# Optimization experiments

Measured on AMD Instinct MI355X. Metric: run time of the kernel, lower is better.

The kernel has to match this reference:

```python
import jax, jax.numpy as jnp
import numpy as np

B, S, D = 2, 2048, 1024
H, DK, DV = 16, 64, 64
D_OUT = 1024


def setup_inputs() -> dict:
    key = jax.random.key(0)
    ks = jax.random.split(key, 9)
    sd = 1.0 / np.sqrt(D)
    # Linear weights stored as [in, out] (torch applies x @ W.T with W [out,in])
    return {
        "x": jax.random.normal(ks[0], (B, S, D), dtype=jnp.float32),
        "Wq": jax.random.normal(ks[1], (D, H * DK), dtype=jnp.float32) * sd,
        "bq": jnp.zeros((H * DK,), dtype=jnp.float32),
        "Wk": jax.random.normal(ks[2], (D, H * DK), dtype=jnp.float32) * sd,
        "bk": jnp.zeros((H * DK,), dtype=jnp.float32),
        "Wv": jax.random.normal(ks[3], (D, H * DV), dtype=jnp.float32) * sd,
        "bv": jnp.zeros((H * DV,), dtype=jnp.float32),
        "Wo": jax.random.normal(ks[4], (H * DV, D_OUT), dtype=jnp.float32) * sd,
        "bo": jnp.zeros((D_OUT,), dtype=jnp.float32),
    }


def _attn(x, Wq, bq, Wk, bk, Wv, bv, Wo, bo):
    n = x.shape[-2]
    q = (x @ Wq + bq).reshape(B, n, H, DK).transpose(0, 2, 1, 3)  # [B,H,S,DK]
    k = (x @ Wk + bk).reshape(B, n, H, DK).transpose(0, 2, 1, 3)
    v = (x @ Wv + bv).reshape(B, n, H, DV).transpose(0, 2, 1, 3)
    scores = jnp.einsum("bhqd,bhkd->bhqk", q / jnp.sqrt(jnp.float32(DK)), k)
    # causal additive mask: 0 on/below diagonal, -inf above (matches 1 - 1/tril)
    causal = jnp.tril(jnp.ones((n, n), dtype=bool))
    scores = jnp.where(causal, scores, -jnp.inf)
    probs = jax.nn.softmax(scores, axis=-1)
    out = jnp.einsum("bhqk,bhkd->bhqd", probs, v)  # [B,H,S,DV]
    out = out.transpose(0, 2, 1, 3).reshape(B, n, H * DV)
    return out @ Wo + bo


def reference(x, Wq, bq, Wk, bk, Wv, bv, Wo, bo):
    return _attn(x, Wq, bq, Wk, bk, Wv, bv, Wo, bo)
```

## Files before the change

### kernel.cpp

```cpp
#include <hip/hip_runtime.h>

typedef unsigned short u16;
typedef __bf16 bf16_t;
typedef bf16_t bf16x8 __attribute__((ext_vector_type(8)));
typedef float f32x4 __attribute__((ext_vector_type(4)));

#define DEV __device__ __forceinline__
#define LOG2E 1.4426950408889634f
#define QKS (0.125f * LOG2E)

static_assert(sizeof(bf16x8) == 16, "bf16x8 must be 16B");

DEV u16 f2b(float v) { return __builtin_bit_cast(u16, (bf16_t)v); }
DEV float b2f(u16 v) { return (float)__builtin_bit_cast(bf16_t, v); }

DEV void g2l16(const void* g, void* l) {
  __builtin_amdgcn_global_load_lds(
      (const __attribute__((address_space(1))) void*)g,
      (__attribute__((address_space(3))) void*)l, 16, 0, 0);
}

DEV int sniff_is_f32(const u16* __restrict__ W) {
  const int lane = threadIdx.x & 63;
  int cnt = 0;
#pragma unroll
  for (int i = 0; i < 8; i++) {
    u16 u = W[(lane * 8 + i) * 2];
    cnt += (((u >> 7) & 0xFF) >= 126) ? 1 : 0;
  }
#pragma unroll
  for (int off = 1; off < 64; off <<= 1) cnt += __shfl_xor(cnt, off, 64);
  return cnt > 128;
}


__global__ __launch_bounds__(256) void convert_x_k(
    const void* __restrict__ xin, const u16* __restrict__ Wsniff,
    u16* __restrict__ xb) {
  const int i = (blockIdx.x * 256 + threadIdx.x) * 8;
  if (sniff_is_f32(Wsniff)) {
    const float* xf = (const float*)xin;
    float4 a = *(const float4*)&xf[i];
    float4 b = *(const float4*)&xf[i + 4];
    u16 o[8] = {f2b(a.x), f2b(a.y), f2b(a.z), f2b(a.w),
                f2b(b.x), f2b(b.y), f2b(b.z), f2b(b.w)};
    *(uint4*)&xb[i] = *(const uint4*)o;
  } else {
    *(uint4*)&xb[i] = *(const uint4*)((const u16*)xin + i);
  }
}

__global__ __launch_bounds__(256) void transpose_k(
    const void* __restrict__ Wq, const void* __restrict__ Wk,
    const void* __restrict__ Wv, const void* __restrict__ Wo,
    const void* __restrict__ bq, const void* __restrict__ bk,
    const void* __restrict__ bv, const void* __restrict__ bo,
    u16* __restrict__ Wqkv_t, u16* __restrict__ Wo_t,
    u16* __restrict__ bqkv_b, u16* __restrict__ bo_b) {
  __shared__ u16 tile[64][68];
  const int z = blockIdx.z;
  const void* src = (z == 0) ? Wq : (z == 1) ? Wk : (z == 2) ? Wv : Wo;
  u16* dst = (z < 3) ? (Wqkv_t + (size_t)z * 1024 * 1024) : Wo_t;
  const int k0 = blockIdx.y * 64, n0 = blockIdx.x * 64;
  const int t = threadIdx.x;
  const int r = t >> 4, c4 = (t & 15) * 4;
  const int isf = sniff_is_f32((const u16*)Wq);

  if (blockIdx.x == 0 && blockIdx.y == 0) {
    const void* bsrc = (z == 0) ? bq : (z == 1) ? bk : (z == 2) ? bv : bo;
    u16* bdst = (z < 3) ? (bqkv_b + z * 1024) : bo_b;
#pragma unroll
    for (int i = 0; i < 4; i++) {
      const int idx = t + i * 256;
      const float v =
          isf ? ((const float*)bsrc)[idx] : b2f(((const u16*)bsrc)[idx]);
      bdst[idx] = f2b(v);
    }
  }

#pragma unroll
  for (int i = 0; i < 4; i++) {
    int rr = r + i * 16;
    const size_t base = (size_t)(k0 + rr) * 1024 + n0 + c4;
    if (isf) {
      float4 v = *(const float4*)((const float*)src + base);
      tile[rr][c4] = f2b(v.x); tile[rr][c4 + 1] = f2b(v.y);
      tile[rr][c4 + 2] = f2b(v.z); tile[rr][c4 + 3] = f2b(v.w);
    } else {
      ushort4 v = *(const ushort4*)((const u16*)src + base);
      tile[rr][c4] = v.x; tile[rr][c4 + 1] = v.y;
      tile[rr][c4 + 2] = v.z; tile[rr][c4 + 3] = v.w;
    }
  }
  __syncthreads();
#pragma unroll
  for (int i = 0; i < 4; i++) {
    int rr = r + i * 16;
    ushort4 v;
    v.x = tile[c4][rr]; v.y = tile[c4 + 1][rr];
    v.z = tile[c4 + 2][rr]; v.w = tile[c4 + 3][rr];
    *(ushort4*)&dst[(size_t)(n0 + rr) * 1024 + k0 + c4] = v;
  }
}

template <int MODE>
__global__ __launch_bounds__(256, 3) void gemm_k(
    const u16* __restrict__ A, const u16* __restrict__ Bt,
    const u16* __restrict__ bias, void* __restrict__ o0v,
    u16* __restrict__ o1, u16* __restrict__ o2,
    const u16* __restrict__ Wsniff, int M, int N, int K) {
  alignas(16) __shared__ u16 As[128][32];
  alignas(16) __shared__ u16 Bs[128][32];
  const int tid = threadIdx.x;
  const int wave = tid >> 6, lane = tid & 63;
  const int quad = lane >> 4, l16 = lane & 15;
  const int m0 = blockIdx.y * 128, n0 = blockIdx.x * 128;
  const int wr = (wave >> 1) * 64, wc = (wave & 1) * 64;

  f32x4 acc[4][4];
#pragma unroll
  for (int i = 0; i < 4; i++)
#pragma unroll
    for (int j = 0; j < 4; j++) acc[i][j] = (f32x4){0.f, 0.f, 0.f, 0.f};

  const int srow = lane >> 2, scol = (lane & 3) * 8;
  for (int k0 = 0; k0 < K; k0 += 32) {
    __syncthreads();
#pragma unroll
    for (int j = 0; j < 4; j++) {
      const int t = wave * 4 + j;
      if (t < 8) {
        const int row = t * 16 + srow;
        g2l16(&A[(size_t)(m0 + row) * K + k0 + scol], &As[t * 16][0]);
      } else {
        const int rb = t - 8;
        const int row = rb * 16 + srow;
        g2l16(&Bt[(size_t)(n0 + row) * K + k0 + scol], &Bs[rb * 16][0]);
      }
    }
    __syncthreads();
    bf16x8 af[4], bfr[4];
#pragma unroll
    for (int mi = 0; mi < 4; mi++)
      af[mi] = *(const bf16x8*)&As[wr + mi * 16 + l16][quad * 8];
#pragma unroll
    for (int ni = 0; ni < 4; ni++)
      bfr[ni] = *(const bf16x8*)&Bs[wc + ni * 16 + l16][quad * 8];
#pragma unroll
    for (int mi = 0; mi < 4; mi++)
#pragma unroll
      for (int ni = 0; ni < 4; ni++)
        acc[mi][ni] = __builtin_amdgcn_mfma_f32_16x16x32_bf16(
            af[mi], bfr[ni], acc[mi][ni], 0, 0, 0);
  }

  const int isf = (MODE == 1) ? sniff_is_f32(Wsniff) : 0;
#pragma unroll
  for (int mi = 0; mi < 4; mi++) {
    const int rbase = m0 + wr + mi * 16 + quad * 4;
#pragma unroll
    for (int ni = 0; ni < 4; ni++) {
      const int col = n0 + wc + ni * 16 + l16;
      const float bv_ = b2f(bias[col]);
      if (MODE == 0) {
        const int seg = col >> 10;
        const int nn = col & 1023;
        const int h = nn >> 6, d = nn & 63;
        u16* op = (seg == 0) ? (u16*)o0v : (seg == 1) ? o1 : o2;
#pragma unroll
        for (int r = 0; r < 4; r++) {
          const int m = rbase + r;
          const int b = m >> 11, s = m & 2047;
          float v = acc[mi][ni][r] + bv_;
          if (seg == 0) v *= QKS;
          if (seg < 2)
            op[(((size_t)(b * 16 + h) * 2048) + s) * 64 + d] = f2b(v);
          else
            op[(((size_t)(b * 16 + h) * 64) + d) * 2048 + s] = f2b(v);
        }
      } else {
#pragma unroll
        for (int r = 0; r < 4; r++) {
          const int m = rbase + r;
          const float v = acc[mi][ni][r] + bv_;
          if (isf) ((float*)o0v)[(size_t)m * N + col] = v;
          else     ((u16*)o0v)[(size_t)m * N + col] = f2b(v);
        }
      }
    }
  }
}

__global__ __launch_bounds__(512, 4) void attn_k(
    const u16* __restrict__ Q, const u16* __restrict__ K,
    const u16* __restrict__ Vt, u16* __restrict__ O) {
  alignas(16) __shared__ u16 Ks[2][128][64];
  alignas(16) __shared__ u16 Vs[2][64][128];
  alignas(16) __shared__ u16 PsT[128][64];
  const int tid = threadIdx.x;
  const int w = tid >> 6, lane = tid & 63;
  const int quad = lane >> 4, l16 = lane & 15;
  const int bh = blockIdx.y;
  const int b = bh >> 4, h = bh & 15;
  const int sw = l16 & 7;

  const int krow_off = lane >> 3, kchunk = lane & 7;
  const int vrow_off = lane >> 4, vchunk = lane & 15;

  for (int pi = 0; pi < 2; pi++) {
    const int qt = pi ? (15 - (int)blockIdx.x) : (int)blockIdx.x;
    const int q0 = qt * 128;
    const int wrow = q0 + w * 16;
    const int nkt = qt + 1;

    bf16x8 aq[2];
#pragma unroll
    for (int kc = 0; kc < 2; kc++)
      aq[kc] = *(const bf16x8*)&Q[((size_t)bh * 2048 + wrow + l16) * 64 +
                                  kc * 32 + quad * 8];

    f32x4 oacc[4];
#pragma unroll
    for (int di = 0; di < 4; di++) oacc[di] = (f32x4){0.f, 0.f, 0.f, 0.f};
    float lrp = 0.f;

    auto stage = [&](int buf, int kts) {
      const int k0s = kts * 128;
#pragma unroll
      for (int j = 0; j < 4; j++) {
        const int t = w * 4 + j;
        if (t < 16) {
          const int r = t * 8 + krow_off;
          const int cs = kchunk ^ (r & 7);
          g2l16(&K[((size_t)bh * 2048 + k0s + r) * 64 + cs * 8],
                &Ks[buf][t * 8][0]);
        } else {
          const int t2 = t - 16;
          const int r = t2 * 4 + vrow_off;
          const int cs = vchunk ^ (r & 7);
          g2l16(&Vt[((size_t)bh * 64 + r) * 2048 + k0s + cs * 8],
                &Vs[buf][t2 * 4][0]);
        }
      }
    };

    stage(0, 0);
    for (int kt = 0; kt < nkt; kt++) {
      const int cur = kt & 1;
      const int k0 = kt * 128;
      if (kt + 1 < nkt) {
        stage(cur ^ 1, kt + 1);
        asm volatile("s_waitcnt vmcnt(4)" ::: "memory");
      } else {
        asm volatile("s_waitcnt vmcnt(0)" ::: "memory");
      }
      asm volatile("s_barrier" ::: "memory");

#pragma unroll
      for (int h2 = 0; h2 < 2; h2++) {
        const int k0h = k0 + h2 * 64;
        if (k0h > wrow + 15) continue;
        const bool needmask = (k0h + 63 > wrow);

        f32x4 st[4];
#pragma unroll
        for (int nk = 0; nk < 4; nk++) st[nk] = (f32x4){0.f, 0.f, 0.f, 0.f};
#pragma unroll
        for (int kc = 0; kc < 2; kc++)
#pragma unroll
          for (int nk = 0; nk < 4; nk++) {
            const int pos = ((kc << 2) | quad) ^ sw;
            bf16x8 kf =
                *(const bf16x8*)&Ks[cur][h2 * 64 + nk * 16 + l16][pos * 8];
            st[nk] = __builtin_amdgcn_mfma_f32_16x16x32_bf16(kf, aq[kc],
                                                             st[nk], 0, 0, 0);
          }

        const int q_glob = wrow + l16;
#pragma unroll
        for (int nk = 0; nk < 4; nk++) {
          const int kbase = k0h + nk * 16 + quad * 4;
          u16 pk[4];
#pragma unroll
          for (int r = 0; r < 4; r++) {
            float p = __builtin_amdgcn_exp2f(st[nk][r]);
            if (needmask && (kbase + r > q_glob)) p = 0.f;
            lrp += p;
            pk[r] = f2b(p);
          }
          const int g = nk * 4 + quad;
          const int cc = (g >> 1) ^ sw;
          *(uint2*)&PsT[w * 16 + l16][cc * 8 + (g & 1) * 4] =
              *(const uint2*)pk;
        }
        asm volatile("s_waitcnt lgkmcnt(0)" ::: "memory");

#pragma unroll
        for (int kc = 0; kc < 2; kc++) {
          const int pcc = ((kc << 2) | quad) ^ sw;
          bf16x8 ap = *(const bf16x8*)&PsT[w * 16 + l16][pcc * 8];
#pragma unroll
          for (int di = 0; di < 4; di++) {
            const int pos = ((h2 << 3) | (kc << 2) | quad) ^ sw;
            bf16x8 vf = *(const bf16x8*)&Vs[cur][di * 16 + l16][pos * 8];
            oacc[di] = __builtin_amdgcn_mfma_f32_16x16x32_bf16(ap, vf,
                                                               oacc[di], 0, 0, 0);
          }
        }
      }
      asm volatile("s_barrier" ::: "memory");
    }

    lrp += __shfl_xor(lrp, 16, 64);
    lrp += __shfl_xor(lrp, 32, 64);
    float rdiv[4];
#pragma unroll
    for (int r = 0; r < 4; r++) rdiv[r] = __shfl(lrp, quad * 4 + r, 64);

#pragma unroll
    for (int di = 0; di < 4; di++)
#pragma unroll
      for (int r = 0; r < 4; r++) {
        const int row = wrow + quad * 4 + r;
        const float v = oacc[di][r] / rdiv[r];
        O[((size_t)b * 2048 + row) * 1024 + h * 64 + di * 16 + l16] = f2b(v);
      }
  }
}

extern "C" void kernel_launch(void* const* d_in, const int* in_sizes, int n_in,
                              void* d_out, int out_size, void* d_ws,
                              size_t ws_size, hipStream_t stream) {
  const void* x  = d_in[0];
  const void* Wq = d_in[1];
  const void* bq = d_in[2];
  const void* Wk = d_in[3];
  const void* bk = d_in[4];
  const void* Wv = d_in[5];
  const void* bv = d_in[6];
  const void* Wo = d_in[7];
  const void* bo = d_in[8];

  char* ws = (char*)d_ws;
  u16* xb     = (u16*)ws;          ws += (size_t)4096 * 1024 * 2;
  u16* Wqkv_t = (u16*)ws;          ws += (size_t)3072 * 1024 * 2;
  u16* Wo_t   = (u16*)ws;          ws += (size_t)1024 * 1024 * 2;
  u16* bqkv_b = (u16*)ws;          ws += 3072 * 2;
  u16* bo_b   = (u16*)ws;          ws += 1024 * 2 + 128;
  u16* Qb     = (u16*)ws;          ws += (size_t)4096 * 1024 * 2;
  u16* Kb     = (u16*)ws;          ws += (size_t)4096 * 1024 * 2;
  u16* Vtb    = (u16*)ws;          ws += (size_t)4096 * 1024 * 2;
  u16* Ob     = xb;

  convert_x_k<<<2048, 256, 0, stream>>>(x, (const u16*)Wq, xb);
  transpose_k<<<dim3(16, 16, 4), 256, 0, stream>>>(Wq, Wk, Wv, Wo, bq, bk, bv,
                                                   bo, Wqkv_t, Wo_t, bqkv_b,
                                                   bo_b);
  gemm_k<0><<<dim3(24, 32), 256, 0, stream>>>(xb, Wqkv_t, bqkv_b, Qb, Kb, Vtb,
                                              (const u16*)Wq, 4096, 3072, 1024);
  attn_k<<<dim3(8, 32), 512, 0, stream>>>(Qb, Kb, Vtb, Ob);
  gemm_k<1><<<dim3(8, 32), 256, 0, stream>>>(Ob, Wo_t, bo_b, d_out, nullptr,
                                             nullptr, (const u16*)Wq, 4096,
                                             1024, 1024);
}
```

Measured before the change: 210.6 us.

## Split attention KV tiles across two blocks, widen GEMM K-step, stage V transpose

The attention kernel now splits each query tile's key tiles between two blocks, alternating even and odd tiles. Each block writes unnormalized partial outputs and row sums, and a new norm kernel combines and normalizes them. This doubles the grid, giving more parallelism for the causal workload, at the cost of an extra kernel launch and extra global traffic for the partials. Separately, the GEMM now uses a 64-wide K step with swizzled LDS, and the V-transposed epilogue is staged through shared memory so the global stores are coalesced.

```diff
diff --git a/kernel.cpp b/kernel.cpp
--- a/kernel.cpp
+++ b/kernel.cpp
@@ -109,13 +109,15 @@
     const u16* __restrict__ bias, void* __restrict__ o0v,
     u16* __restrict__ o1, u16* __restrict__ o2,
     const u16* __restrict__ Wsniff, int M, int N, int K) {
-  alignas(16) __shared__ u16 As[128][32];
-  alignas(16) __shared__ u16 Bs[128][32];
+  alignas(16) __shared__ u16 smem[2][128][64];
+  u16(*As)[64] = smem[0];
+  u16(*Bs)[64] = smem[1];
   const int tid = threadIdx.x;
   const int wave = tid >> 6, lane = tid & 63;
   const int quad = lane >> 4, l16 = lane & 15;
   const int m0 = blockIdx.y * 128, n0 = blockIdx.x * 128;
   const int wr = (wave >> 1) * 64, wc = (wave & 1) * 64;
+  const int sw = l16 & 7;
 
   f32x4 acc[4][4];
 #pragma unroll
@@ -123,35 +125,76 @@
 #pragma unroll
     for (int j = 0; j < 4; j++) acc[i][j] = (f32x4){0.f, 0.f, 0.f, 0.f};
 
-  const int srow = lane >> 2, scol = (lane & 3) * 8;
-  for (int k0 = 0; k0 < K; k0 += 32) {
+  const int srow = lane >> 3, schunk = lane & 7;
+  const int cs = schunk ^ srow;
+
+  for (int k0 = 0; k0 < K; k0 += 64) {
     __syncthreads();
 #pragma unroll
-    for (int j = 0; j < 4; j++) {
-      const int t = wave * 4 + j;
-      if (t < 8) {
-        const int row = t * 16 + srow;
-        g2l16(&A[(size_t)(m0 + row) * K + k0 + scol], &As[t * 16][0]);
+    for (int j = 0; j < 8; j++) {
+      const int t = wave * 8 + j;
+      if (t < 16) {
+        const int row = t * 8 + srow;
+        g2l16(&A[(size_t)(m0 + row) * K + k0 + cs * 8], &As[t * 8][0]);
       } else {
-        const int rb = t - 8;
-        const int row = rb * 16 + srow;
-        g2l16(&Bt[(size_t)(n0 + row) * K + k0 + scol], &Bs[rb * 16][0]);
+        const int t2 = t - 16;
+        const int row = t2 * 8 + srow;
+        g2l16(&Bt[(size_t)(n0 + row) * K + k0 + cs * 8], &Bs[t2 * 8][0]);
       }
     }
     __syncthreads();
-    bf16x8 af[4], bfr[4];
-#pragma unroll
-    for (int mi = 0; mi < 4; mi++)
-      af[mi] = *(const bf16x8*)&As[wr + mi * 16 + l16][quad * 8];
-#pragma unroll
-    for (int ni = 0; ni < 4; ni++)
-      bfr[ni] = *(const bf16x8*)&Bs[wc + ni * 16 + l16][quad * 8];
-#pragma unroll
-    for (int mi = 0; mi < 4; mi++)
+#pragma unroll
+    for (int kk = 0; kk < 2; kk++) {
+      const int pos = ((kk << 2) | quad) ^ sw;
+      bf16x8 af[4], bfr[4];
+#pragma unroll
+      for (int mi = 0; mi < 4; mi++)
+        af[mi] = *(const bf16x8*)&As[wr + mi * 16 + l16][pos * 8];
 #pragma unroll
       for (int ni = 0; ni < 4; ni++)
-        acc[mi][ni] = __builtin_amdgcn_mfma_f32_16x16x32_bf16(
-            af[mi], bfr[ni], acc[mi][ni], 0, 0, 0);
+        bfr[ni] = *(const bf16x8*)&Bs[wc + ni * 16 + l16][pos * 8];
+#pragma unroll
+      for (int mi = 0; mi < 4; mi++)
+#pragma unroll
+        for (int ni = 0; ni < 4; ni++)
+          acc[mi][ni] = __builtin_amdgcn_mfma_f32_16x16x32_bf16(
+              af[mi], bfr[ni], acc[mi][ni], 0, 0, 0);
+    }
+  }
+
+  if (MODE == 0 && n0 >= 2048) {
+    u16* T = &smem[0][0][0];
+    const int b = m0 >> 11, sb = m0 & 2047;
+#pragma unroll
+    for (int r2 = 0; r2 < 2; r2++) {
+      __syncthreads();
+      if (wc == r2 * 64) {
+#pragma unroll
+        for (int mi = 0; mi < 4; mi++)
+#pragma unroll
+          for (int ni = 0; ni < 4; ni++) {
+            const int c = ni * 16 + l16;
+            const int col = n0 + r2 * 64 + c;
+            const float bv_ = b2f(bias[col]);
+#pragma unroll
+            for (int r = 0; r < 4; r++) {
+              const int s = wr + mi * 16 + quad * 4 + r;
+              T[c * 136 + s] = f2b(acc[mi][ni][r] + bv_);
+            }
+          }
+      }
+      __syncthreads();
+      {
+        const int c = tid >> 2, s8 = (tid & 3) * 32;
+        const int nn = (n0 - 2048) + r2 * 64 + c;
+        const int h = nn >> 6, d = nn & 63;
+        u16* dst = &o2[(((size_t)(b * 16 + h) * 64) + d) * 2048 + sb];
+#pragma unroll
+        for (int j2 = 0; j2 < 4; j2++)
+          *(uint4*)&dst[s8 + j2 * 8] = *(const uint4*)&T[c * 136 + s8 + j2 * 8];
+      }
+    }
+    return;
   }
 
   const int isf = (MODE == 1) ? sniff_is_f32(Wsniff) : 0;
@@ -166,17 +209,14 @@
         const int seg = col >> 10;
         const int nn = col & 1023;
         const int h = nn >> 6, d = nn & 63;
-        u16* op = (seg == 0) ? (u16*)o0v : (seg == 1) ? o1 : o2;
+        u16* op = (seg == 0) ? (u16*)o0v : o1;
 #pragma unroll
         for (int r = 0; r < 4; r++) {
           const int m = rbase + r;
           const int b = m >> 11, s = m & 2047;
           float v = acc[mi][ni][r] + bv_;
           if (seg == 0) v *= QKS;
-          if (seg < 2)
-            op[(((size_t)(b * 16 + h) * 2048) + s) * 64 + d] = f2b(v);
-          else
-            op[(((size_t)(b * 16 + h) * 64) + d) * 2048 + s] = f2b(v);
+          op[(((size_t)(b * 16 + h) * 2048) + s) * 64 + d] = f2b(v);
         }
       } else {
 #pragma unroll
@@ -193,25 +233,32 @@
 
 __global__ __launch_bounds__(512, 4) void attn_k(
     const u16* __restrict__ Q, const u16* __restrict__ K,
-    const u16* __restrict__ Vt, u16* __restrict__ O) {
+    const u16* __restrict__ Vt, u16* __restrict__ p0, u16* __restrict__ p1,
+    float* __restrict__ l0, float* __restrict__ l1) {
   alignas(16) __shared__ u16 Ks[2][128][64];
   alignas(16) __shared__ u16 Vs[2][64][128];
   alignas(16) __shared__ u16 PsT[128][64];
   const int tid = threadIdx.x;
   const int w = tid >> 6, lane = tid & 63;
   const int quad = lane >> 4, l16 = lane & 15;
+  const int split = blockIdx.x & 1;
+  const int pairIdx = blockIdx.x >> 1;
   const int bh = blockIdx.y;
   const int b = bh >> 4, h = bh & 15;
   const int sw = l16 & 7;
 
+  u16* Op = split ? p1 : p0;
+  float* lp = split ? l1 : l0;
+
   const int krow_off = lane >> 3, kchunk = lane & 7;
   const int vrow_off = lane >> 4, vchunk = lane & 15;
 
   for (int pi = 0; pi < 2; pi++) {
-    const int qt = pi ? (15 - (int)blockIdx.x) : (int)blockIdx.x;
+    const int qt = pi ? (15 - pairIdx) : pairIdx;
     const int q0 = qt * 128;
     const int wrow = q0 + w * 16;
     const int nkt = qt + 1;
+    const int cnt = (nkt - split + 1) >> 1;
 
     bf16x8 aq[2];
 #pragma unroll
@@ -244,12 +291,12 @@
       }
     };
 
-    stage(0, 0);
-    for (int kt = 0; kt < nkt; kt++) {
-      const int cur = kt & 1;
-      const int k0 = kt * 128;
-      if (kt + 1 < nkt) {
-        stage(cur ^ 1, kt + 1);
+    if (cnt > 0) stage(0, split);
+    for (int ti = 0; ti < cnt; ti++) {
+      const int cur = ti & 1;
+      const int k0 = (split + 2 * ti) * 128;
+      if (ti + 1 < cnt) {
+        stage(cur ^ 1, split + 2 * (ti + 1));
         asm volatile("s_waitcnt vmcnt(4)" ::: "memory");
       } else {
         asm volatile("s_waitcnt vmcnt(0)" ::: "memory");
@@ -303,8 +350,8 @@
           for (int di = 0; di < 4; di++) {
             const int pos = ((h2 << 3) | (kc << 2) | quad) ^ sw;
             bf16x8 vf = *(const bf16x8*)&Vs[cur][di * 16 + l16][pos * 8];
-            oacc[di] = __builtin_amdgcn_mfma_f32_16x16x32_bf16(ap, vf,
-                                                               oacc[di], 0, 0, 0);
+            oacc[di] = __builtin_amdgcn_mfma_f32_16x16x32_bf16(
+                ap, vf, oacc[di], 0, 0, 0);
           }
         }
       }
@@ -313,19 +360,38 @@
 
     lrp += __shfl_xor(lrp, 16, 64);
     lrp += __shfl_xor(lrp, 32, 64);
-    float rdiv[4];
-#pragma unroll
-    for (int r = 0; r < 4; r++) rdiv[r] = __shfl(lrp, quad * 4 + r, 64);
+    if (lane < 16) lp[(size_t)bh * 2048 + wrow + lane] = lrp;
 
 #pragma unroll
     for (int di = 0; di < 4; di++)
 #pragma unroll
       for (int r = 0; r < 4; r++) {
         const int row = wrow + quad * 4 + r;
-        const float v = oacc[di][r] / rdiv[r];
-        O[((size_t)b * 2048 + row) * 1024 + h * 64 + di * 16 + l16] = f2b(v);
-      }
-  }
+        Op[((size_t)b * 2048 + row) * 1024 + h * 64 + di * 16 + l16] =
+            f2b(oacc[di][r]);
+      }
+  }
+}
+
+__global__ __launch_bounds__(256) void norm_k(
+    const u16* __restrict__ p0, const u16* __restrict__ p1,
+    const float* __restrict__ l0, const float* __restrict__ l1,
+    u16* __restrict__ out) {
+  const int i = (blockIdx.x * 256 + threadIdx.x) * 8;
+  const int row = i >> 10;
+  const int col = i & 1023;
+  const int bh = ((row >> 11) << 4) | (col >> 6);
+  const int q = row & 2047;
+  const size_t li = (size_t)bh * 2048 + q;
+  const float rc = 1.0f / (l0[li] + l1[li]);
+  uint4 a = *(const uint4*)&p0[i];
+  uint4 bb = *(const uint4*)&p1[i];
+  const u16* au = (const u16*)&a;
+  const u16* bu = (const u16*)&bb;
+  u16 o[8];
+#pragma unroll
+  for (int j = 0; j < 8; j++) o[j] = f2b((b2f(au[j]) + b2f(bu[j])) * rc);
+  *(uint4*)&out[i] = *(const uint4*)o;
 }
 
 extern "C" void kernel_launch(void* const* d_in, const int* in_sizes, int n_in,
@@ -350,6 +416,10 @@
   u16* Qb     = (u16*)ws;          ws += (size_t)4096 * 1024 * 2;
   u16* Kb     = (u16*)ws;          ws += (size_t)4096 * 1024 * 2;
   u16* Vtb    = (u16*)ws;          ws += (size_t)4096 * 1024 * 2;
+  u16* p1     = (u16*)ws;          ws += (size_t)4096 * 1024 * 2;
+  float* l0   = (float*)ws;        ws += (size_t)32 * 2048 * 4;
+  float* l1   = (float*)ws;        ws += (size_t)32 * 2048 * 4;
+  u16* p0     = xb;
   u16* Ob     = xb;
 
   convert_x_k<<<2048, 256, 0, stream>>>(x, (const u16*)Wq, xb);
@@ -358,7 +428,8 @@
                                                    bo_b);
   gemm_k<0><<<dim3(24, 32), 256, 0, stream>>>(xb, Wqkv_t, bqkv_b, Qb, Kb, Vtb,
                                               (const u16*)Wq, 4096, 3072, 1024);
-  attn_k<<<dim3(8, 32), 512, 0, stream>>>(Qb, Kb, Vtb, Ob);
+  attn_k<<<dim3(16, 32), 512, 0, stream>>>(Qb, Kb, Vtb, p0, p1, l0, l1);
+  norm_k<<<2048, 256, 0, stream>>>(p0, p1, l0, l1, Ob);
   gemm_k<1><<<dim3(8, 32), 256, 0, stream>>>(Ob, Wo_t, bo_b, d_out, nullptr,
                                              nullptr, (const u16*)Wq, 4096,
                                              1024, 1024);
```

New measurement: 199.2 us. 5.4% less time.
